# Kernel optimization log

Hardware: AMD Instinct MI355X
Metric: run time of the kernel (lower is better)

Reference implementation:

```python
import jax, jax.numpy as jnp
import numpy as np

EPS = 1e-5


def _bn(x, gamma, beta, axes, ch_shape):
    # training-mode batch norm: stats over `axes`, affine over channel dim
    mean = jnp.mean(x, axis=axes, keepdims=True)
    var = jnp.var(x, axis=axes, keepdims=True)
    xn = (x - mean) * jax.lax.rsqrt(var + EPS)
    return xn * gamma.reshape(ch_shape) + beta.reshape(ch_shape)


def setup_inputs() -> dict:
    key = jax.random.key(0)
    ks = jax.random.split(key, 5)
    b, d, n1, n2 = 32, 256, 32, 32
    k_dim, h, v = 16, 4, 64  # d == h * v
    n = n1 * n2
    m = n  # global context
    std_kv = 1.0 / np.sqrt(d)
    std_q = 1.0 / np.sqrt(d * k_dim)
    return {
        "x": jax.random.normal(ks[0], (b, d, n1, n2), jnp.float32),
        "Wq": jax.random.normal(ks[1], (k_dim * h, d), jnp.float32) * std_q,
        "Wk": jax.random.normal(ks[2], (k_dim, d), jnp.float32) * std_kv,
        "Wv": jax.random.normal(ks[3], (v, d), jnp.float32) * std_kv,
        "E": jax.random.normal(ks[4], (n, m, k_dim), jnp.float32),
        "gamma_v": jnp.ones((m,), jnp.float32),
        "beta_v": jnp.zeros((m,), jnp.float32),
        "gamma_q": jnp.ones((k_dim,), jnp.float32),
        "beta_q": jnp.zeros((k_dim,), jnp.float32),
    }


def reference(x, Wq, Wk, Wv, E, gamma_v, beta_v, gamma_q, beta_q):
    b, d, n1, n2 = x.shape
    n = n1 * n2
    k_dim = Wk.shape[0]
    h = Wq.shape[0] // k_dim
    xf = x.reshape(b, n, d)          # [b, n, d]; c == xf since m == n
    keys = xf @ Wk.T                 # [b, m, k]
    softmax_keys = jax.nn.softmax(keys, axis=1)
    values = _bn(xf @ Wv.T, gamma_v, beta_v, axes=(0, 2), ch_shape=(1, -1, 1))  # [b, m, v]
    queries = (xf @ Wq.T).reshape(b, n, k_dim, h).transpose(0, 2, 1, 3)          # [b, k, n, h]
    queries = _bn(queries, gamma_q, beta_q, axes=(0, 2, 3), ch_shape=(1, -1, 1, 1))
    content_lambda = jnp.einsum('bmk,bmv->bkv', softmax_keys, values)
    position_lambdas = jnp.einsum('nmk,bmv->bnkv', E, values)
    content_output = jnp.einsum('bknh,bkv->bhvn', queries, content_lambda)
    position_output = jnp.einsum('bknh,bnkv->bhvn', queries, position_lambdas)
    return (content_output + position_output).reshape(b, d, n1, n2)
```

## Files before the change

kernel.cpp:

```cpp
#include <hip/hip_runtime.h>
#include <math.h>


#define BB 32
#define DD 256
#define NPOS 1024
#define KDIM 16
#define HH 4
#define VV 64
#define F_EPS 1e-5f

#define NBLK 8
#define TMM 64

typedef __attribute__((ext_vector_type(8))) short short8;
typedef __attribute__((ext_vector_type(4))) float f32x4;
typedef unsigned short ushort_t;
typedef unsigned int uint_t;

typedef __attribute__((address_space(1))) const uint_t g32_t;
typedef __attribute__((address_space(3))) uint_t l32_t;

__device__ __forceinline__ void gload16(const void* g, void* l) {
    __builtin_amdgcn_global_load_lds((g32_t*)g, (l32_t*)l, 16, 0, 0);
}

__device__ __forceinline__ uint_t bfpack(float x, float y) {
    uint_t ux = __float_as_uint(x), uy = __float_as_uint(y);
    ux = (ux + 0x7FFFu + ((ux >> 16) & 1u)) >> 16;
    uy = (uy + 0x7FFFu + ((uy >> 16) & 1u)) >> 16;
    return ux | (uy << 16);
}
__device__ __forceinline__ ushort_t f2bf(float x) {
    uint_t u = __float_as_uint(x);
    return (ushort_t)((u + 0x7FFFu + ((u >> 16) & 1u)) >> 16);
}
__device__ __forceinline__ float bflo(uint_t u) { return __uint_as_float(u << 16); }
__device__ __forceinline__ float bfhi(uint_t u) { return __uint_as_float(u & 0xFFFF0000u); }

__global__ void k_wcvt(const float* __restrict__ Wq, const float* __restrict__ Wk,
                       const float* __restrict__ Wv, ushort_t* __restrict__ Wb) {
    int i = blockIdx.x*256 + threadIdx.x;
    int fi = i*8;
    int row = fi >> 8, col = fi & 255;
    const float* src;
    if (row < 16)      src = Wk + row*DD + col;
    else if (row < 80) src = Wv + (row-16)*DD + col;
    else               src = Wq + (row-80)*DD + col;
    float4 a = ((const float4*)src)[0], c = ((const float4*)src)[1];
    uint4 o;
    o.x = bfpack(a.x, a.y); o.y = bfpack(a.z, a.w);
    o.z = bfpack(c.x, c.y); o.w = bfpack(c.z, c.w);
    *(uint4*)(Wb + fi) = o;
}

__global__ __launch_bounds__(256) void k_projm(
        const float* __restrict__ x, const ushort_t* __restrict__ Wb,
        float* __restrict__ keys, float* __restrict__ vals, float* __restrict__ qrs) {
    const int b = blockIdx.x, nt = blockIdx.y;
    const int w = threadIdx.x >> 6, lane = threadIdx.x & 63;
    const int l15 = lane & 15, l4 = lane >> 4;
    const int n = nt*64 + w*16 + l15;

    const float* xr = x + ((size_t)b*NPOS + n)*DD + l4*8;
    float4 xa[8][2];
    #pragma unroll
    for (int ks = 0; ks < 8; ++ks) {
        xa[ks][0] = *(const float4*)(xr + ks*32);
        xa[ks][1] = *(const float4*)(xr + ks*32 + 4);
    }

    f32x4 acc[9];
    #pragma unroll
    for (int m = 0; m < 9; ++m) acc[m] = (f32x4){0.f,0.f,0.f,0.f};

    const ushort_t* wp = Wb + (size_t)l15*DD + l4*8;
    #pragma unroll
    for (int ks = 0; ks < 8; ++ks) {
        union { uint_t u[4]; short8 s8; } bu;
        bu.u[0] = bfpack(xa[ks][0].x, xa[ks][0].y);
        bu.u[1] = bfpack(xa[ks][0].z, xa[ks][0].w);
        bu.u[2] = bfpack(xa[ks][1].x, xa[ks][1].y);
        bu.u[3] = bfpack(xa[ks][1].z, xa[ks][1].w);
        #pragma unroll
        for (int m = 0; m < 9; ++m) {
            short8 wf = *(const short8*)(wp + (size_t)m*16*DD + ks*32);
            acc[m] = __builtin_amdgcn_mfma_f32_16x16x32_bf16(wf, bu.s8, acc[m], 0, 0, 0);
        }
    }

    #pragma unroll
    for (int m = 0; m < 9; ++m) {
        float* dst;
        int c0 = m*16 + l4*4;
        if (m == 0)      dst = keys + (size_t)b*KDIM*NPOS + (size_t)c0*NPOS;
        else if (m < 5)  dst = vals + (size_t)b*VV*NPOS   + (size_t)(c0-16)*NPOS;
        else             dst = qrs  + (size_t)b*VV*NPOS   + (size_t)(c0-80)*NPOS;
        #pragma unroll
        for (int i = 0; i < 4; ++i)
            dst[(size_t)i*NPOS + n] = acc[m][i];
    }
}

__global__ void k_zero(float* __restrict__ p, int nfl) {
    int i = blockIdx.x * 256 + threadIdx.x;
    if (i < nfl) p[i] = 0.f;
}

__global__ void k_ecvt(const float* __restrict__ E, ushort_t* __restrict__ Eb) {
    size_t i = (size_t)blockIdx.x * 256 + threadIdx.x;
    const float4* s = (const float4*)(E + i*8);
    float4 a = s[0], c = s[1];
    uint4 o;
    o.x = bfpack(a.x, a.y); o.y = bfpack(a.z, a.w);
    o.z = bfpack(c.x, c.y); o.w = bfpack(c.z, c.w);
    *(uint4*)(Eb + i*8) = o;
}

__global__ void k_softmax(float* __restrict__ keys) {
    const int wid  = (blockIdx.x * 256 + threadIdx.x) >> 6;
    const int lane = threadIdx.x & 63;
    float* row = keys + (size_t)wid * NPOS;
    float v[16];
    float mx = -1e30f;
    #pragma unroll
    for (int j = 0; j < 16; ++j) { v[j] = row[lane + 64*j]; mx = fmaxf(mx, v[j]); }
    #pragma unroll
    for (int off = 32; off >= 1; off >>= 1) mx = fmaxf(mx, __shfl_xor(mx, off));
    float s = 0.f;
    #pragma unroll
    for (int j = 0; j < 16; ++j) { v[j] = __expf(v[j] - mx); s += v[j]; }
    #pragma unroll
    for (int off = 32; off >= 1; off >>= 1) s += __shfl_xor(s, off);
    float inv = 1.f / s;
    #pragma unroll
    for (int j = 0; j < 16; ++j) row[lane + 64*j] = v[j] * inv;
}

__global__ void k_vstats(const float* __restrict__ vals, float* __restrict__ sv) {
    const int g = blockIdx.x, t = threadIdx.x;
    float s[4] = {0,0,0,0}, q[4] = {0,0,0,0};
    for (int r = g*32; r < g*32 + 32; ++r) {
        const float* row = vals + (size_t)r * NPOS;
        #pragma unroll
        for (int j = 0; j < 4; ++j) { float x = row[t + 256*j]; s[j] += x; q[j] += x*x; }
    }
    #pragma unroll
    for (int j = 0; j < 4; ++j) {
        atomicAdd(&sv[t + 256*j], s[j]);
        atomicAdd(&sv[1024 + t + 256*j], q[j]);
    }
}

__global__ void k_vfinal(float* __restrict__ sv, const float* __restrict__ gv,
                         const float* __restrict__ bv) {
    int m = blockIdx.x*256 + threadIdx.x;
    float mean = sv[m] * (1.f/2048.f);
    float var  = sv[1024+m] * (1.f/2048.f) - mean*mean;
    float sc = rsqrtf(var + F_EPS) * gv[m];
    sv[m] = sc;
    sv[1024+m] = bv[m] - mean*sc;
}

__global__ void k_vcvt(const float* __restrict__ vals, const float* __restrict__ sv,
                       ushort_t* __restrict__ vb) {
    int i = blockIdx.x*256 + threadIdx.x;
    int m0 = (i & 127) * 8;
    const float4* src = (const float4*)(vals + (size_t)i*8);
    float4 a = src[0], c = src[1];
    float4 s0 = *(const float4*)(sv + m0),        s1 = *(const float4*)(sv + m0 + 4);
    float4 h0 = *(const float4*)(sv + 1024 + m0), h1 = *(const float4*)(sv + 1024 + m0 + 4);
    a.x = a.x*s0.x + h0.x; a.y = a.y*s0.y + h0.y; a.z = a.z*s0.z + h0.z; a.w = a.w*s0.w + h0.w;
    c.x = c.x*s1.x + h1.x; c.y = c.y*s1.y + h1.y; c.z = c.z*s1.z + h1.z; c.w = c.w*s1.w + h1.w;
    uint4 o;
    o.x = bfpack(a.x, a.y); o.y = bfpack(a.z, a.w);
    o.z = bfpack(c.x, c.y); o.w = bfpack(c.z, c.w);
    *(uint4*)(vb + (size_t)i*8) = o;
}

__global__ void k_qstats(const float* __restrict__ qrs, float* __restrict__ sq) {
    const int kd = blockIdx.x >> 3, sub = blockIdx.x & 7;
    float s = 0.f, ss = 0.f;
    for (int b = sub*4; b < sub*4 + 4; ++b)
        for (int h = 0; h < HH; ++h) {
            const float* row = qrs + ((size_t)(b*KDIM*HH) + kd*4 + h) * NPOS;
            #pragma unroll
            for (int j = 0; j < 4; ++j) { float x = row[threadIdx.x + 256*j]; s += x; ss += x*x; }
        }
    #pragma unroll
    for (int off = 32; off >= 1; off >>= 1) { s += __shfl_xor(s, off); ss += __shfl_xor(ss, off); }
    __shared__ float red[8];
    int w = threadIdx.x >> 6, lane = threadIdx.x & 63;
    if (lane == 0) { red[w] = s; red[4+w] = ss; }
    __syncthreads();
    if (threadIdx.x == 0) atomicAdd(&sq[kd],    red[0]+red[1]+red[2]+red[3]);
    if (threadIdx.x == 1) atomicAdd(&sq[16+kd], red[4]+red[5]+red[6]+red[7]);
}

__global__ void k_qfinal(float* __restrict__ sq, const float* __restrict__ gq,
                         const float* __restrict__ bq) {
    int kd = threadIdx.x;
    const float inv = 1.f / 131072.f;
    float mean = sq[kd] * inv;
    float var  = sq[16+kd] * inv - mean*mean;
    float sc = rsqrtf(var + F_EPS) * gq[kd];
    sq[kd] = sc;
    sq[16+kd] = bq[kd] - mean*sc;
}

__global__ void k_qT(const float* __restrict__ qrs, const float* __restrict__ sq,
                     ushort_t* __restrict__ qb) {
    __shared__ float tile[64][68];
    const int b = blockIdx.x >> 4, n0 = (blockIdx.x & 15) * 64;
    const int t = threadIdx.x;
    {
        int c = t >> 2, j0 = t & 3;
        const float4* src = (const float4*)(qrs + ((size_t)b*64 + c)*NPOS + n0);
        #pragma unroll
        for (int i = 0; i < 4; ++i) {
            float4 v = src[j0 + i*4];
            *(float4*)&tile[c][(j0 + i*4)*4] = v;
        }
    }
    __syncthreads();
    int n_l = t >> 2, h = t & 3;
    float q16[16];
    #pragma unroll
    for (int kd = 0; kd < 16; ++kd)
        q16[kd] = tile[kd*4 + h][n_l] * sq[kd] + sq[16 + kd];
    uint4 lo, hi, z;
    lo.x = bfpack(q16[0], q16[1]);  lo.y = bfpack(q16[2], q16[3]);
    lo.z = bfpack(q16[4], q16[5]);  lo.w = bfpack(q16[6], q16[7]);
    hi.x = bfpack(q16[8], q16[9]);  hi.y = bfpack(q16[10], q16[11]);
    hi.z = bfpack(q16[12], q16[13]); hi.w = bfpack(q16[14], q16[15]);
    z.x = z.y = z.z = z.w = 0u;
    ushort_t* dst = qb + (size_t)b*131072 + (size_t)((n0 + n_l)*4 + h)*32;
    *(uint4*)(dst)      = lo;
    *(uint4*)(dst + 8)  = hi;
    *(uint4*)(dst + 16) = z;
    *(uint4*)(dst + 24) = z;
}

__global__ void k_cl(const float* __restrict__ sk, const ushort_t* __restrict__ vb,
                     ushort_t* __restrict__ clb) {
    const int b = blockIdx.x >> 4, kd = blockIdx.x & 15;
    __shared__ float skl[NPOS];
    __shared__ float red[256];
    const int t = threadIdx.x;
    const float* srow = sk + ((size_t)b*KDIM + kd) * NPOS;
    #pragma unroll
    for (int j = 0; j < 4; ++j) skl[t + 256*j] = srow[t + 256*j];
    __syncthreads();
    const int v = t >> 2, q = t & 3;
    const uint4* v4 = (const uint4*)(vb + ((size_t)b*VV + v) * NPOS + q*256);
    const float4* s4 = (const float4*)(skl + q*256);
    float s = 0.f;
    #pragma unroll 8
    for (int m8 = 0; m8 < 32; ++m8) {
        uint4 wv = v4[m8];
        float4 sa = s4[m8*2], sb = s4[m8*2+1];
        s += sa.x*bflo(wv.x) + sa.y*bfhi(wv.x) + sa.z*bflo(wv.y) + sa.w*bfhi(wv.y)
           + sb.x*bflo(wv.z) + sb.y*bfhi(wv.z) + sb.z*bflo(wv.w) + sb.w*bfhi(wv.w);
    }
    red[t] = s;
    __syncthreads();
    if (q == 0) {
        float r = red[t] + red[t+1] + red[t+2] + red[t+3];
        clb[((size_t)b*VV + v)*16 + kd] = f2bf(r);
    }
}

__global__ __launch_bounds__(256) void k_main(
        const ushort_t* __restrict__ qb, const ushort_t* __restrict__ vb,
        const ushort_t* __restrict__ Eb, const ushort_t* __restrict__ clb,
        float* __restrict__ out) {
    __shared__ ushort_t E_lds[2][NBLK][TMM][16];
    __shared__ ushort_t vb_lds[2][VV][TMM];
    __shared__ ushort_t A_lds[32][TMM];

    const int wg  = blockIdx.x;
    const int b   = (wg >> 3) & 31;
    const int g   = (wg & 7) * 16 + (wg >> 8);
    const int n0  = g * NBLK;
    const int t   = threadIdx.x;
    const int w   = t >> 6, lane = t & 63;
    const int l15 = lane & 15, l4 = lane >> 4;

    char* Ab = (char*)&A_lds[0][0];

    const int mw = w & 1, vf0 = (w >> 1) * 2;

    short8 qf[2];
    #pragma unroll
    for (int j = 0; j < 2; ++j) {
        const ushort_t* qp = qb + ((size_t)b*131072)
                           + (size_t)((n0 + w*2 + j)*4 + l15)*32 + l4*8;
        qf[j] = *(const short8*)qp;
    }

    const ushort_t* vb_b = vb + (size_t)b*VV*NPOS;

    #define STAGE(mt, bufi) do {                                                  \
        const int m0_ = (mt) * TMM;                                               \
        _Pragma("unroll")                                                         \
        for (int qq = 0; qq < 4; ++qq) {                                          \
            int flat = w*4 + qq, nn_ = flat >> 1, half_ = flat & 1;               \
            const ushort_t* src = Eb + ((size_t)(n0+nn_)*NPOS + m0_)*16           \
                                   + half_*512 + lane*8;                          \
            gload16(src, &E_lds[bufi][nn_][half_*32][0]);                         \
        }                                                                         \
        _Pragma("unroll")                                                         \
        for (int qq = 0; qq < 2; ++qq) {                                          \
            int slot = (w*2 + qq)*64 + lane;                                      \
            int v_ = slot >> 3, cs_ = slot & 7, c_ = cs_ ^ (v_ & 7);              \
            const ushort_t* src = vb_b + (size_t)v_*NPOS + m0_ + c_*8;            \
            gload16(src, (char*)&vb_lds[bufi][0][0] + (w*2 + qq)*1024);           \
        }                                                                         \
    } while (0)

    STAGE(0, 0);
    asm volatile("s_waitcnt vmcnt(0)" ::: "memory");
    __syncthreads();

    f32x4 acc[2];
    acc[0] = (f32x4){0.f,0.f,0.f,0.f};
    acc[1] = (f32x4){0.f,0.f,0.f,0.f};

    int buf = 0;
    for (int mt = 0; mt < NPOS/TMM; ++mt) {
        if (mt < NPOS/TMM - 1) STAGE(mt + 1, buf ^ 1);

        f32x4 aacc[8];
        #pragma unroll
        for (int j = 0; j < 2; ++j) {
            #pragma unroll
            for (int mf = 0; mf < 4; ++mf) {
                short8 e = *(const short8*)&E_lds[buf][w*2 + j][mf*16 + l15][(l4 & 1)*8];
                aacc[j*4 + mf] = __builtin_amdgcn_mfma_f32_16x16x32_bf16(
                    e, qf[j], (f32x4){0.f,0.f,0.f,0.f}, 0, 0, 0);
            }
        }
        __syncthreads();

        if (l15 < 4) {
            #pragma unroll
            for (int j = 0; j < 2; ++j) {
                int arow = (w*2 + j)*4 + l15;
                int sw = (arow & 7) << 4;
                #pragma unroll
                for (int mf = 0; mf < 4; ++mf) {
                    f32x4 a = aacc[j*4 + mf];
                    int byte = (arow*128 + mf*32 + l4*8) ^ sw;
                    *(uint2*)(Ab + byte) = make_uint2(bfpack(a[0], a[1]), bfpack(a[2], a[3]));
                }
            }
        }
        __syncthreads();

        #pragma unroll
        for (int s = 0; s < 2; ++s) {
            int arow = mw*16 + l15;
            int abyte = (arow*128 + s*64 + l4*16) ^ ((arow & 7) << 4);
            short8 af = *(const short8*)(Ab + abyte);
            #pragma unroll
            for (int nf = 0; nf < 2; ++nf) {
                int v_ = (vf0 + nf)*16 + l15;
                int vbyte = (v_*128 + (s*4 + l4)*16) ^ ((v_ & 7) << 4);
                short8 bfr = *(const short8*)((char*)&vb_lds[buf][0][0] + vbyte);
                acc[nf] = __builtin_amdgcn_mfma_f32_16x16x32_bf16(af, bfr, acc[nf], 0, 0, 0);
            }
        }

        asm volatile("s_waitcnt vmcnt(0)" ::: "memory");
        __syncthreads();
        buf ^= 1;
    }

    {
        const ushort_t* qa = qb + (size_t)b*131072
                           + (size_t)(n0*4 + mw*16 + l15)*32 + l4*8;
        short8 aq = *(const short8*)qa;
        #pragma unroll
        for (int nf = 0; nf < 2; ++nf) {
            const ushort_t* cb = clb + ((size_t)b*VV + (vf0 + nf)*16 + l15)*16 + l4*8;
            short8 bq = *(const short8*)cb;
            acc[nf] = __builtin_amdgcn_mfma_f32_16x16x32_bf16(aq, bq, acc[nf], 0, 0, 0);
        }
    }

    #pragma unroll
    for (int nf = 0; nf < 2; ++nf) {
        int v_ = (vf0 + nf)*16 + l15;
        int r0 = mw*16 + l4*4;
        int nn = r0 >> 2;
        #pragma unroll
        for (int i = 0; i < 4; ++i) {
            out[(((size_t)b*HH + i)*VV + v_)*NPOS + n0 + nn] = acc[nf][i];
        }
    }
    #undef STAGE
}

extern "C" void kernel_launch(void* const* d_in, const int* in_sizes, int n_in,
                              void* d_out, int out_size, void* d_ws, size_t ws_size,
                              hipStream_t stream) {
    const float* x  = (const float*)d_in[0];
    const float* Wq = (const float*)d_in[1];
    const float* Wk = (const float*)d_in[2];
    const float* Wv = (const float*)d_in[3];
    const float* E  = (const float*)d_in[4];
    const float* gv = (const float*)d_in[5];
    const float* bv = (const float*)d_in[6];
    const float* gq = (const float*)d_in[7];
    const float* bq = (const float*)d_in[8];
    float* out = (float*)d_out;

    float* ws   = (float*)d_ws;
    float* keys = ws;
    float* vals = keys + 524288;
    float* qrs  = vals + 2097152;
    float* sv   = qrs  + 2097152;
    float* sq   = sv   + 2048;
    ushort_t* cl_bf = (ushort_t*)(sq + 32);
    ushort_t* q_bf  = cl_bf + 32832;
    ushort_t* vb_bf = q_bf  + 4196352;
    ushort_t* E_bf  = vb_bf + 2097152;
    ushort_t* W_bf  = E_bf  + 16777216;

    k_zero<<<9, 256, 0, stream>>>(sv, 2048 + 32);
    k_wcvt<<<18, 256, 0, stream>>>(Wq, Wk, Wv, W_bf);
    k_projm<<<dim3(BB, 16), 256, 0, stream>>>(x, W_bf, keys, vals, qrs);
    k_ecvt<<<8192, 256, 0, stream>>>(E, E_bf);
    k_softmax<<<128, 256, 0, stream>>>(keys);
    k_vstats<<<64, 256, 0, stream>>>(vals, sv);
    k_vfinal<<<4, 256, 0, stream>>>(sv, gv, bv);
    k_vcvt<<<1024, 256, 0, stream>>>(vals, sv, vb_bf);
    k_qstats<<<128, 256, 0, stream>>>(qrs, sq);
    k_qfinal<<<1, 16, 0, stream>>>(sq, gq, bq);
    k_qT<<<512, 256, 0, stream>>>(qrs, sq, q_bf);
    k_cl<<<512, 256, 0, stream>>>(keys, vb_bf, cl_bf);
    k_main<<<4096, 256, 0, stream>>>(q_bf, vb_bf, E_bf, cl_bf, out);
}
```

Before: 344.9 us.

## Restructure main loop barriers, hoist staging addresses, and add MFMA priority hints

The per-iteration schedule moves the wait-for-loads plus barrier to the top of the loop, before the next tile's prefetch is issued. This cuts the three block-wide barriers per iteration to two, and the middle one becomes a raw s_barrier after an LDS waitcnt. Global source pointers and LDS offsets for the E and v staging are computed once and advanced by increments, replacing full recomputation each tile. The MFMA phases are wrapped in s_setprio, and the loop is unrolled by 4. The aim is less synchronization and address arithmetic per tile, at the cost of a more fragile hand-built ordering of barriers and waitcnts.

```diff
diff --git a/kernel.cpp b/kernel.cpp
--- a/kernel.cpp
+++ b/kernel.cpp
@@ -286,7 +286,9 @@
     const int w   = t >> 6, lane = t & 63;
     const int l15 = lane & 15, l4 = lane >> 4;
 
-    char* Ab = (char*)&A_lds[0][0];
+    char* Ab    = (char*)&A_lds[0][0];
+    char* Ebase = (char*)&E_lds[0][0][0][0];
+    char* Vbase = (char*)&vb_lds[0][0][0];
 
     const int mw = w & 1, vf0 = (w >> 1) * 2;
 
@@ -299,37 +301,51 @@
     }
 
     const ushort_t* vb_b = vb + (size_t)b*VV*NPOS;
-
-    #define STAGE(mt, bufi) do {                                                  \
-        const int m0_ = (mt) * TMM;                                               \
-        _Pragma("unroll")                                                         \
-        for (int qq = 0; qq < 4; ++qq) {                                          \
-            int flat = w*4 + qq, nn_ = flat >> 1, half_ = flat & 1;               \
-            const ushort_t* src = Eb + ((size_t)(n0+nn_)*NPOS + m0_)*16           \
-                                   + half_*512 + lane*8;                          \
-            gload16(src, &E_lds[bufi][nn_][half_*32][0]);                         \
-        }                                                                         \
-        _Pragma("unroll")                                                         \
-        for (int qq = 0; qq < 2; ++qq) {                                          \
-            int slot = (w*2 + qq)*64 + lane;                                      \
-            int v_ = slot >> 3, cs_ = slot & 7, c_ = cs_ ^ (v_ & 7);              \
-            const ushort_t* src = vb_b + (size_t)v_*NPOS + m0_ + c_*8;            \
-            gload16(src, (char*)&vb_lds[bufi][0][0] + (w*2 + qq)*1024);           \
-        }                                                                         \
+    const ushort_t* eSrc[4]; uint_t eOffB[4];
+    #pragma unroll
+    for (int qq = 0; qq < 4; ++qq) {
+        int flat = w*4 + qq, nn_ = flat >> 1, half_ = flat & 1;
+        eSrc[qq]  = Eb + ((size_t)(n0+nn_)*NPOS)*16 + half_*512 + lane*8;
+        eOffB[qq] = nn_*2048u + half_*1024u;
+    }
+    const ushort_t* vSrc[2]; uint_t vOffB[2];
+    #pragma unroll
+    for (int qq = 0; qq < 2; ++qq) {
+        int slot = (w*2 + qq)*64 + lane;
+        int v_ = slot >> 3, cs_ = slot & 7, c_ = cs_ ^ (v_ & 7);
+        vSrc[qq]  = vb_b + (size_t)v_*NPOS + c_*8;
+        vOffB[qq] = (w*2 + qq)*1024u;
+    }
+
+    #define STAGE2(bufsel) do {                                        \
+        _Pragma("unroll")                                              \
+        for (int qq = 0; qq < 4; ++qq) {                               \
+            gload16(eSrc[qq], Ebase + (bufsel)*16384u + eOffB[qq]);    \
+            eSrc[qq] += 1024;                                          \
+        }                                                              \
+        _Pragma("unroll")                                              \
+        for (int qq = 0; qq < 2; ++qq) {                               \
+            gload16(vSrc[qq], Vbase + (bufsel)*8192u + vOffB[qq]);     \
+            vSrc[qq] += 64;                                            \
+        }                                                              \
     } while (0)
 
-    STAGE(0, 0);
-    asm volatile("s_waitcnt vmcnt(0)" ::: "memory");
-    __syncthreads();
+    STAGE2(0);
 
     f32x4 acc[2];
     acc[0] = (f32x4){0.f,0.f,0.f,0.f};
     acc[1] = (f32x4){0.f,0.f,0.f,0.f};
 
     int buf = 0;
+    #pragma unroll 4
     for (int mt = 0; mt < NPOS/TMM; ++mt) {
-        if (mt < NPOS/TMM - 1) STAGE(mt + 1, buf ^ 1);
-
+        asm volatile("s_waitcnt vmcnt(0)" ::: "memory");
+        __builtin_amdgcn_s_barrier();
+        asm volatile("" ::: "memory");
+
+        if (mt < NPOS/TMM - 1) STAGE2(buf ^ 1);
+
+        __builtin_amdgcn_s_setprio(1);
         f32x4 aacc[8];
         #pragma unroll
         for (int j = 0; j < 2; ++j) {
@@ -340,7 +356,7 @@
                     e, qf[j], (f32x4){0.f,0.f,0.f,0.f}, 0, 0, 0);
             }
         }
-        __syncthreads();
+        __builtin_amdgcn_s_setprio(0);
 
         if (l15 < 4) {
             #pragma unroll
@@ -355,8 +371,11 @@
                 }
             }
         }
-        __syncthreads();
-
+        asm volatile("s_waitcnt lgkmcnt(0)" ::: "memory");
+        __builtin_amdgcn_s_barrier();
+        asm volatile("" ::: "memory");
+
+        __builtin_amdgcn_s_setprio(1);
         #pragma unroll
         for (int s = 0; s < 2; ++s) {
             int arow = mw*16 + l15;
@@ -370,9 +389,7 @@
                 acc[nf] = __builtin_amdgcn_mfma_f32_16x16x32_bf16(af, bfr, acc[nf], 0, 0, 0);
             }
         }
-
-        asm volatile("s_waitcnt vmcnt(0)" ::: "memory");
-        __syncthreads();
+        __builtin_amdgcn_s_setprio(0);
         buf ^= 1;
     }
 
@@ -398,7 +415,7 @@
             out[(((size_t)b*HH + i)*VV + v_)*NPOS + n0 + nn] = acc[nf][i];
         }
     }
-    #undef STAGE
+    #undef STAGE2
 }
 
 extern "C" void kernel_launch(void* const* d_in, const int* in_sizes, int n_in,
```

Measured after the change: 337.9 us. 1.02x faster.

## Restructure position-lambda kernel with pre-swizzled E layout and register-resident E tiles

Applied to the files above, without the earlier changes.

Converts E into a layout matched to the MFMA fragment order, so the main kernel loads E straight into registers instead of staging it through LDS. Queries are written as block-diagonal, zero-padded fragments so each wave computes its 4 n×4 h products with two chained MFMAs. The intermediate is then repacked in registers and fed directly into the V MFMA, which removes the A_lds round trip and two barriers per tile. E loads are software-pipelined with ping-pong registers, and the MFMA section runs under s_setprio. In exchange the query buffer grows to hold the padded blocks, register pressure rises, and wasted MFMA work on the zero padding increases.

```diff
diff --git a/kernel.cpp b/kernel.cpp
--- a/kernel.cpp
+++ b/kernel.cpp
@@ -10,10 +10,8 @@
 #define VV 64
 #define F_EPS 1e-5f
 
-#define NBLK 8
-#define TMM 64
-
 typedef __attribute__((ext_vector_type(8))) short short8;
+typedef __attribute__((ext_vector_type(4))) short s16x4;
 typedef __attribute__((ext_vector_type(4))) float f32x4;
 typedef unsigned short ushort_t;
 typedef unsigned int uint_t;
@@ -37,6 +35,20 @@
 }
 __device__ __forceinline__ float bflo(uint_t u) { return __uint_as_float(u << 16); }
 __device__ __forceinline__ float bfhi(uint_t u) { return __uint_as_float(u & 0xFFFF0000u); }
+
+#define MFMA32(a,b,c) __builtin_amdgcn_mfma_f32_16x16x32_bf16(a,b,c,0,0,0)
+
+__device__ __forceinline__ s16x4 pack4(f32x4 p) {
+    union { uint_t u[2]; s16x4 s; } r;
+    r.u[0] = bfpack(p[0], p[1]);
+    r.u[1] = bfpack(p[2], p[3]);
+    return r.s;
+}
+__device__ __forceinline__ short8 cat4(s16x4 a, s16x4 b) {
+    union { s16x4 h[2]; short8 v; } r;
+    r.h[0] = a; r.h[1] = b;
+    return r.v;
+}
 
 __global__ void k_wcvt(const float* __restrict__ Wq, const float* __restrict__ Wk,
                        const float* __restrict__ Wv, ushort_t* __restrict__ Wb) {
@@ -85,7 +97,7 @@
         #pragma unroll
         for (int m = 0; m < 9; ++m) {
             short8 wf = *(const short8*)(wp + (size_t)m*16*DD + ks*32);
-            acc[m] = __builtin_amdgcn_mfma_f32_16x16x32_bf16(wf, bu.s8, acc[m], 0, 0, 0);
+            acc[m] = MFMA32(wf, bu.s8, acc[m]);
         }
     }
 
@@ -107,14 +119,21 @@
     if (i < nfl) p[i] = 0.f;
 }
 
-__global__ void k_ecvt(const float* __restrict__ E, ushort_t* __restrict__ Eb) {
-    size_t i = (size_t)blockIdx.x * 256 + threadIdx.x;
-    const float4* s = (const float4*)(E + i*8);
-    float4 a = s[0], c = s[1];
+__global__ void k_ecvt2(const float* __restrict__ E, ushort_t* __restrict__ E2) {
+    size_t C = (size_t)blockIdx.x * 256 + threadIdx.x;
+    int c8 = (int)(C & 511);
+    size_t T = C >> 9;
+    int m  = c8 >> 3, s = (c8 >> 2) & 1, l4c = c8 & 3;
+    int mt = (int)(T & 15);
+    int ncg = (int)(T >> 4);
+    int n = ncg*4 + s*2 + (l4c >> 1);
+    int kd0 = (l4c & 1) * 8;
+    const float* src = E + ((size_t)n*NPOS + mt*64 + m)*KDIM + kd0;
+    float4 a = ((const float4*)src)[0], c = ((const float4*)src)[1];
     uint4 o;
     o.x = bfpack(a.x, a.y); o.y = bfpack(a.z, a.w);
     o.z = bfpack(c.x, c.y); o.w = bfpack(c.z, c.w);
-    *(uint4*)(Eb + i*8) = o;
+    *(uint4*)(E2 + C*8) = o;
 }
 
 __global__ void k_softmax(float* __restrict__ keys) {
@@ -209,13 +228,13 @@
 }
 
 __global__ void k_qT(const float* __restrict__ qrs, const float* __restrict__ sq,
-                     ushort_t* __restrict__ qb) {
+                     ushort_t* __restrict__ qd, ushort_t* __restrict__ qc) {
     __shared__ float tile[64][68];
-    const int b = blockIdx.x >> 4, n0 = (blockIdx.x & 15) * 64;
+    const int b = blockIdx.x >> 4, nt = blockIdx.x & 15;
     const int t = threadIdx.x;
     {
         int c = t >> 2, j0 = t & 3;
-        const float4* src = (const float4*)(qrs + ((size_t)b*64 + c)*NPOS + n0);
+        const float4* src = (const float4*)(qrs + ((size_t)b*64 + c)*NPOS + nt*64);
         #pragma unroll
         for (int i = 0; i < 4; ++i) {
             float4 v = src[j0 + i*4];
@@ -223,22 +242,37 @@
         }
     }
     __syncthreads();
-    int n_l = t >> 2, h = t & 3;
+    const int ncg_l = t >> 4, col = t & 15;
+    const int ncg = nt*16 + ncg_l;
+    const int n_local = ncg_l*4 + (col >> 2), h = col & 3;
     float q16[16];
     #pragma unroll
     for (int kd = 0; kd < 16; ++kd)
-        q16[kd] = tile[kd*4 + h][n_l] * sq[kd] + sq[16 + kd];
-    uint4 lo, hi, z;
-    lo.x = bfpack(q16[0], q16[1]);  lo.y = bfpack(q16[2], q16[3]);
-    lo.z = bfpack(q16[4], q16[5]);  lo.w = bfpack(q16[6], q16[7]);
-    hi.x = bfpack(q16[8], q16[9]);  hi.y = bfpack(q16[10], q16[11]);
-    hi.z = bfpack(q16[12], q16[13]); hi.w = bfpack(q16[14], q16[15]);
-    z.x = z.y = z.z = z.w = 0u;
-    ushort_t* dst = qb + (size_t)b*131072 + (size_t)((n0 + n_l)*4 + h)*32;
-    *(uint4*)(dst)      = lo;
-    *(uint4*)(dst + 8)  = hi;
-    *(uint4*)(dst + 16) = z;
-    *(uint4*)(dst + 24) = z;
+        q16[kd] = tile[kd*4 + h][n_local] * sq[kd] + sq[16 + kd];
+
+    {
+        uint_t wv[8];
+        #pragma unroll
+        for (int w2 = 0; w2 < 8; ++w2) wv[w2] = bfpack(q16[2*w2], q16[2*w2+1]);
+        uint4* dst = (uint4*)(qc + (((size_t)b*256 + ncg)*16 + col)*16);
+        dst[0] = make_uint4(wv[0], wv[1], wv[2], wv[3]);
+        dst[1] = make_uint4(wv[4], wv[5], wv[6], wv[7]);
+    }
+    #pragma unroll
+    for (int s = 0; s < 2; ++s) {
+        uint_t wv[16];
+        #pragma unroll
+        for (int w2 = 0; w2 < 16; ++w2) {
+            int nlk = w2 >> 3;
+            int kd = (2*w2) & 15;
+            wv[w2] = ((col >> 2) == s*2 + nlk) ? bfpack(q16[kd], q16[kd+1]) : 0u;
+        }
+        uint4* dst = (uint4*)(qd + ((((size_t)b*256 + ncg)*2 + s)*16 + col)*32);
+        dst[0] = make_uint4(wv[0],  wv[1],  wv[2],  wv[3]);
+        dst[1] = make_uint4(wv[4],  wv[5],  wv[6],  wv[7]);
+        dst[2] = make_uint4(wv[8],  wv[9],  wv[10], wv[11]);
+        dst[3] = make_uint4(wv[12], wv[13], wv[14], wv[15]);
+    }
 }
 
 __global__ void k_cl(const float* __restrict__ sk, const ushort_t* __restrict__ vb,
@@ -271,134 +305,119 @@
 }
 
 __global__ __launch_bounds__(256) void k_main(
-        const ushort_t* __restrict__ qb, const ushort_t* __restrict__ vb,
-        const ushort_t* __restrict__ Eb, const ushort_t* __restrict__ clb,
-        float* __restrict__ out) {
-    __shared__ ushort_t E_lds[2][NBLK][TMM][16];
-    __shared__ ushort_t vb_lds[2][VV][TMM];
-    __shared__ ushort_t A_lds[32][TMM];
+        const ushort_t* __restrict__ qd, const ushort_t* __restrict__ qc,
+        const ushort_t* __restrict__ clb, const ushort_t* __restrict__ vb,
+        const ushort_t* __restrict__ E2, float* __restrict__ out) {
+    __shared__ ushort_t vb_lds[2][VV][64];
 
     const int wg  = blockIdx.x;
     const int b   = (wg >> 3) & 31;
     const int g   = (wg & 7) * 16 + (wg >> 8);
-    const int n0  = g * NBLK;
+    const int n0  = g * 8;
     const int t   = threadIdx.x;
     const int w   = t >> 6, lane = t & 63;
     const int l15 = lane & 15, l4 = lane >> 4;
-
-    char* Ab = (char*)&A_lds[0][0];
-
-    const int mw = w & 1, vf0 = (w >> 1) * 2;
-
-    short8 qf[2];
-    #pragma unroll
-    for (int j = 0; j < 2; ++j) {
-        const ushort_t* qp = qb + ((size_t)b*131072)
-                           + (size_t)((n0 + w*2 + j)*4 + l15)*32 + l4*8;
-        qf[j] = *(const short8*)qp;
-    }
+    const int cg  = w & 1, vf0 = (w >> 1) << 1;
+    const int ncg = g*2 + cg;
+    const int swz = (l15 & 7) << 4;
+
+    char* VBc = (char*)&vb_lds[0][0][0];
+    char* VBw = VBc + (w*2)*1024;
+
+    short8 qd0 = *(const short8*)(qd + ((((size_t)b*256 + ncg)*2 + 0)*16 + l15)*32 + l4*8);
+    short8 qd1 = *(const short8*)(qd + ((((size_t)b*256 + ncg)*2 + 1)*16 + l15)*32 + l4*8);
+    s16x4 qcf  = *(const s16x4*)(qc + (((size_t)b*256 + ncg)*16 + l15)*16 + l4*4);
+    s16x4 clf0 = *(const s16x4*)(clb + ((size_t)b*VV + vf0*16 + l15)*16 + l4*4);
+    s16x4 clf1 = *(const s16x4*)(clb + ((size_t)b*VV + (vf0+1)*16 + l15)*16 + l4*4);
+
+    const ushort_t* ep = E2 + (size_t)ncg*65536 + l15*64 + l4*8;
 
     const ushort_t* vb_b = vb + (size_t)b*VV*NPOS;
-
-    #define STAGE(mt, bufi) do {                                                  \
-        const int m0_ = (mt) * TMM;                                               \
-        _Pragma("unroll")                                                         \
-        for (int qq = 0; qq < 4; ++qq) {                                          \
-            int flat = w*4 + qq, nn_ = flat >> 1, half_ = flat & 1;               \
-            const ushort_t* src = Eb + ((size_t)(n0+nn_)*NPOS + m0_)*16           \
-                                   + half_*512 + lane*8;                          \
-            gload16(src, &E_lds[bufi][nn_][half_*32][0]);                         \
-        }                                                                         \
-        _Pragma("unroll")                                                         \
-        for (int qq = 0; qq < 2; ++qq) {                                          \
-            int slot = (w*2 + qq)*64 + lane;                                      \
-            int v_ = slot >> 3, cs_ = slot & 7, c_ = cs_ ^ (v_ & 7);              \
-            const ushort_t* src = vb_b + (size_t)v_*NPOS + m0_ + c_*8;            \
-            gload16(src, (char*)&vb_lds[bufi][0][0] + (w*2 + qq)*1024);           \
-        }                                                                         \
+    const ushort_t* vS0; const ushort_t* vS1;
+    {
+        int slot0 = (w*2)*64 + lane, slot1 = slot0 + 64;
+        int v0_ = slot0 >> 3, c0_ = (slot0 & 7) ^ (v0_ & 7);
+        int v1_ = slot1 >> 3, c1_ = (slot1 & 7) ^ (v1_ & 7);
+        vS0 = vb_b + (size_t)v0_*NPOS + c0_*8;
+        vS1 = vb_b + (size_t)v1_*NPOS + c1_*8;
+    }
+
+    #define ELOAD(dst, mtv) do {                                          \
+        const ushort_t* _e = ep + (size_t)(mtv)*4096;                     \
+        _Pragma("unroll")                                                 \
+        for (int _mf = 0; _mf < 4; ++_mf) {                               \
+            dst[_mf*2+0] = *(const short8*)(_e + _mf*1024);               \
+            dst[_mf*2+1] = *(const short8*)(_e + _mf*1024 + 32);          \
+        }                                                                 \
     } while (0)
 
-    STAGE(0, 0);
-    asm volatile("s_waitcnt vmcnt(0)" ::: "memory");
-    __syncthreads();
-
-    f32x4 acc[2];
-    acc[0] = (f32x4){0.f,0.f,0.f,0.f};
-    acc[1] = (f32x4){0.f,0.f,0.f,0.f};
-
-    int buf = 0;
-    for (int mt = 0; mt < NPOS/TMM; ++mt) {
-        if (mt < NPOS/TMM - 1) STAGE(mt + 1, buf ^ 1);
-
-        f32x4 aacc[8];
-        #pragma unroll
-        for (int j = 0; j < 2; ++j) {
-            #pragma unroll
-            for (int mf = 0; mf < 4; ++mf) {
-                short8 e = *(const short8*)&E_lds[buf][w*2 + j][mf*16 + l15][(l4 & 1)*8];
-                aacc[j*4 + mf] = __builtin_amdgcn_mfma_f32_16x16x32_bf16(
-                    e, qf[j], (f32x4){0.f,0.f,0.f,0.f}, 0, 0, 0);
-            }
+    #define VSTAGE(mtv, bufsel) do {                                      \
+        gload16(vS0 + (mtv)*64, VBw + (bufsel)*8192);                     \
+        gload16(vS1 + (mtv)*64, VBw + (bufsel)*8192 + 1024);              \
+    } while (0)
+
+    f32x4 acc0 = (f32x4){0.f,0.f,0.f,0.f};
+    f32x4 acc1 = (f32x4){0.f,0.f,0.f,0.f};
+
+    const int row0 = vf0*16 + l15, row1 = (vf0+1)*16 + l15;
+
+    #define ITER(eC, eN, mtv, BUF, PF) do {                                    \
+        asm volatile("s_waitcnt vmcnt(0)" ::: "memory");                       \
+        __builtin_amdgcn_s_barrier();                                          \
+        if (PF) { ELOAD(eN, (mtv)+1); VSTAGE((mtv)+1, (BUF)^1); }              \
+        __builtin_amdgcn_s_setprio(1);                                         \
+        _Pragma("unroll")                                                      \
+        for (int mp = 0; mp < 2; ++mp) {                                       \
+            f32x4 P0 = (f32x4){0.f,0.f,0.f,0.f};                               \
+            P0 = MFMA32(eC[mp*4+0], qd0, P0);                                  \
+            P0 = MFMA32(eC[mp*4+1], qd1, P0);                                  \
+            f32x4 P1 = (f32x4){0.f,0.f,0.f,0.f};                               \
+            P1 = MFMA32(eC[mp*4+2], qd0, P1);                                  \
+            P1 = MFMA32(eC[mp*4+3], qd1, P1);                                  \
+            short8 pb8 = cat4(pack4(P0), pack4(P1));                           \
+            int byA = (mp*64 + l4*8) ^ swz, byB = (mp*64 + 32 + l4*8) ^ swz;   \
+            short8 av0 = cat4(                                                 \
+                *(const s16x4*)(VBc + (BUF)*8192 + row0*128 + byA),            \
+                *(const s16x4*)(VBc + (BUF)*8192 + row0*128 + byB));           \
+            short8 av1 = cat4(                                                 \
+                *(const s16x4*)(VBc + (BUF)*8192 + row1*128 + byA),            \
+                *(const s16x4*)(VBc + (BUF)*8192 + row1*128 + byB));           \
+            acc0 = MFMA32(av0, pb8, acc0);                                     \
+            acc1 = MFMA32(av1, pb8, acc1);                                     \
+        }                                                                      \
+        __builtin_amdgcn_s_setprio(0);                                         \
+    } while (0)
+
+    short8 eA[8], eB[8];
+    ELOAD(eA, 0);
+    VSTAGE(0, 0);
+
+    #pragma unroll 1
+    for (int mt = 0; mt < 16; mt += 2) {
+        ITER(eA, eB, mt,     0, 1);
+        ITER(eB, eA, mt + 1, 1, (mt < 14));
+    }
+
+    {
+        s16x4 z4 = (s16x4){0,0,0,0};
+        short8 qc8 = cat4(qcf, z4);
+        acc0 = MFMA32(cat4(clf0, clf0), qc8, acc0);
+        acc1 = MFMA32(cat4(clf1, clf1), qc8, acc1);
+    }
+
+    {
+        const int h = l15 & 3;
+        const int n = n0 + cg*4 + (l15 >> 2);
+        #pragma unroll
+        for (int i = 0; i < 4; ++i) {
+            int v0_ = vf0*16 + l4*4 + i;
+            out[(((size_t)b*HH + h)*VV + v0_)*NPOS + n]      = acc0[i];
+            out[(((size_t)b*HH + h)*VV + v0_ + 16)*NPOS + n] = acc1[i];
         }
-        __syncthreads();
-
-        if (l15 < 4) {
-            #pragma unroll
-            for (int j = 0; j < 2; ++j) {
-                int arow = (w*2 + j)*4 + l15;
-                int sw = (arow & 7) << 4;
-                #pragma unroll
-                for (int mf = 0; mf < 4; ++mf) {
-                    f32x4 a = aacc[j*4 + mf];
-                    int byte = (arow*128 + mf*32 + l4*8) ^ sw;
-                    *(uint2*)(Ab + byte) = make_uint2(bfpack(a[0], a[1]), bfpack(a[2], a[3]));
-                }
-            }
-        }
-        __syncthreads();
-
-        #pragma unroll
-        for (int s = 0; s < 2; ++s) {
-            int arow = mw*16 + l15;
-            int abyte = (arow*128 + s*64 + l4*16) ^ ((arow & 7) << 4);
-            short8 af = *(const short8*)(Ab + abyte);
-            #pragma unroll
-            for (int nf = 0; nf < 2; ++nf) {
-                int v_ = (vf0 + nf)*16 + l15;
-                int vbyte = (v_*128 + (s*4 + l4)*16) ^ ((v_ & 7) << 4);
-                short8 bfr = *(const short8*)((char*)&vb_lds[buf][0][0] + vbyte);
-                acc[nf] = __builtin_amdgcn_mfma_f32_16x16x32_bf16(af, bfr, acc[nf], 0, 0, 0);
-            }
-        }
-
-        asm volatile("s_waitcnt vmcnt(0)" ::: "memory");
-        __syncthreads();
-        buf ^= 1;
-    }
-
-    {
-        const ushort_t* qa = qb + (size_t)b*131072
-                           + (size_t)(n0*4 + mw*16 + l15)*32 + l4*8;
-        short8 aq = *(const short8*)qa;
-        #pragma unroll
-        for (int nf = 0; nf < 2; ++nf) {
-            const ushort_t* cb = clb + ((size_t)b*VV + (vf0 + nf)*16 + l15)*16 + l4*8;
-            short8 bq = *(const short8*)cb;
-            acc[nf] = __builtin_amdgcn_mfma_f32_16x16x32_bf16(aq, bq, acc[nf], 0, 0, 0);
-        }
-    }
-
-    #pragma unroll
-    for (int nf = 0; nf < 2; ++nf) {
-        int v_ = (vf0 + nf)*16 + l15;
-        int r0 = mw*16 + l4*4;
-        int nn = r0 >> 2;
-        #pragma unroll
-        for (int i = 0; i < 4; ++i) {
-            out[(((size_t)b*HH + i)*VV + v_)*NPOS + n0 + nn] = acc[nf][i];
-        }
-    }
-    #undef STAGE
+    }
+    #undef ITER
+    #undef VSTAGE
+    #undef ELOAD
 }
 
 extern "C" void kernel_launch(void* const* d_in, const int* in_sizes, int n_in,
@@ -421,23 +440,24 @@
     float* qrs  = vals + 2097152;
     float* sv   = qrs  + 2097152;
     float* sq   = sv   + 2048;
-    ushort_t* cl_bf = (ushort_t*)(sq + 32);
-    ushort_t* q_bf  = cl_bf + 32832;
-    ushort_t* vb_bf = q_bf  + 4196352;
-    ushort_t* E_bf  = vb_bf + 2097152;
-    ushort_t* W_bf  = E_bf  + 16777216;
+    ushort_t* clb = (ushort_t*)(sq + 32);
+    ushort_t* qd  = clb + 32832;
+    ushort_t* qc  = qd  + 8388608;
+    ushort_t* vbb = qc  + 2097152;
+    ushort_t* E2  = vbb + 2097152;
+    ushort_t* Wb  = E2  + 16777216;
 
     k_zero<<<9, 256, 0, stream>>>(sv, 2048 + 32);
-    k_wcvt<<<18, 256, 0, stream>>>(Wq, Wk, Wv, W_bf);
-    k_projm<<<dim3(BB, 16), 256, 0, stream>>>(x, W_bf, keys, vals, qrs);
-    k_ecvt<<<8192, 256, 0, stream>>>(E, E_bf);
+    k_wcvt<<<18, 256, 0, stream>>>(Wq, Wk, Wv, Wb);
+    k_projm<<<dim3(BB, 16), 256, 0, stream>>>(x, Wb, keys, vals, qrs);
+    k_ecvt2<<<8192, 256, 0, stream>>>(E, E2);
     k_softmax<<<128, 256, 0, stream>>>(keys);
     k_vstats<<<64, 256, 0, stream>>>(vals, sv);
     k_vfinal<<<4, 256, 0, stream>>>(sv, gv, bv);
-    k_vcvt<<<1024, 256, 0, stream>>>(vals, sv, vb_bf);
+    k_vcvt<<<1024, 256, 0, stream>>>(vals, sv, vbb);
     k_qstats<<<128, 256, 0, stream>>>(qrs, sq);
     k_qfinal<<<1, 16, 0, stream>>>(sq, gq, bq);
-    k_qT<<<512, 256, 0, stream>>>(qrs, sq, q_bf);
-    k_cl<<<512, 256, 0, stream>>>(keys, vb_bf, cl_bf);
-    k_main<<<4096, 256, 0, stream>>>(q_bf, vb_bf, E_bf, cl_bf, out);
-}
+    k_qT<<<512, 256, 0, stream>>>(qrs, sq, qd, qc);
+    k_cl<<<512, 256, 0, stream>>>(keys, vbb, clb);
+    k_main<<<4096, 256, 0, stream>>>(qd, qc, clb, vbb, E2, out);
+}
```

Result: slower. 455.9 us (+32.2%).
